# Performance work log

Hardware: AMD Instinct MI355X
Metric: run time of the kernel (lower is better)

The kernel has to match this reference:

```python
import jax, jax.numpy as jnp
import numpy as np

ALPHA = 0.1
BETA = 1.1
NUM_CLASSES = 16
EPS = 1e-8  # matches torch cosine_similarity eps
BATCH = 131072
DIM = 512


def setup_inputs() -> dict:
    key = jax.random.key(0)
    k1, k2 = jax.random.split(key)
    embeddings = jax.random.normal(k1, (BATCH, DIM), dtype=jnp.float32)
    labels = jax.random.randint(k2, (BATCH,), 0, NUM_CLASSES)
    return {"embeddings": embeddings, "labels": labels}


def _cos_dist(a, b):
    # a: [M, D], b: [N, D] -> 1 - cosine_similarity, shape [M, N]
    an = a / jnp.maximum(jnp.linalg.norm(a, axis=-1, keepdims=True), EPS)
    bn = b / jnp.maximum(jnp.linalg.norm(b, axis=-1, keepdims=True), EPS)
    return 1.0 - an @ bn.T


def reference(embeddings, labels):
    C = NUM_CLASSES
    N = embeddings.shape[0]
    dt = embeddings.dtype

    # class centroids (dummy anchors) via scatter-mean
    cnt = jax.ops.segment_sum(jnp.ones((N,), dt), labels, num_segments=C)  # [C]
    sums = jax.ops.segment_sum(embeddings, labels, num_segments=C)        # [C, D]
    centroids = sums / jnp.maximum(cnt, 1.0)[:, None]
    present = cnt > 0

    # close class pairs: i < j, both present, centroid distance <= beta
    pd = _cos_dist(centroids, centroids)                    # [C, C]
    upper = jnp.triu(jnp.ones((C, C), bool), k=1)
    pairmask = upper & (pd <= BETA) & present[:, None] & present[None, :]
    pm = pairmask.astype(dt)
    deg = pm.sum(1) + pm.sum(0)                             # pairs involving each class

    # distances from every centroid to every sample
    D = _cos_dist(centroids, embeddings)                    # [C, N]

    # intra: each sample of class c contributes relu(d(cent_c, x) - alpha),
    # once per close pair involving c
    d_own = D[labels, jnp.arange(N)]                        # [N]
    intra_sum = jnp.sum(deg[labels] * jax.nn.relu(d_own - ALPHA))

    # inter: S[c, c'] = sum over samples with label c' of relu(beta - d(cent_c, x))
    S = jax.ops.segment_sum(jax.nn.relu(BETA - D).T, labels, num_segments=C).T  # [C, C]
    inter_sum = jnp.sum(pm * (S + S.T))

    # number of terms in each loss list: sum over pairs of (cnt_i + cnt_j)
    count = jnp.sum(deg * cnt)
    denom = jnp.maximum(count, 1.0)
    num_pairs = pm.sum()

    loss = jnp.where(num_pairs > 0, intra_sum / denom + inter_sum / denom, 0.0)
    return loss
```

## Files before the change

kernel.cpp:

```cpp
#include <hip/hip_runtime.h>

constexpr float kAlpha = 0.1f;
constexpr float kBeta  = 1.1f;
constexpr int   kC     = 16;
constexpr int   kD     = 512;
constexpr float kEps   = 1e-8f;

constexpr int SUMS_OFF = 0;
constexpr int CNT_OFF  = 8192;
constexpr int TOT_OFF  = 8208;
constexpr int CN_OFF   = 8224;
constexpr int MSK_OFF  = 16416;
constexpr int SCL_OFF  = 16432;
constexpr int ZERO_FLOATS = 8209;

__global__ __launch_bounds__(512) void k1_sums(const float* __restrict__ emb,
                                               const int* __restrict__ labels,
                                               float* __restrict__ sums,
                                               float* __restrict__ cnt,
                                               int N, int rpb) {
    int tid = threadIdx.x;
    int myc = tid & 15;
    float acc[kC];
#pragma unroll
    for (int c = 0; c < kC; ++c) acc[c] = 0.f;
    float cacc = 0.f;

    int r0 = blockIdx.x * rpb;
    int r1 = min(r0 + rpb, N);
    int r = r0;
    for (; r + 8 <= r1; r += 8) {
        int4 la = *(const int4*)(labels + r);
        int4 lb = *(const int4*)(labels + r + 4);
        const float* e = emb + (size_t)r * kD + tid;
        float v0 = e[0 * kD];
        float v1 = e[1 * kD];
        float v2 = e[2 * kD];
        float v3 = e[3 * kD];
        float v4 = e[4 * kD];
        float v5 = e[5 * kD];
        float v6 = e[6 * kD];
        float v7 = e[7 * kD];
#pragma unroll
        for (int c = 0; c < kC; ++c) {
            float s = (la.x == c ? v0 : 0.f) + (la.y == c ? v1 : 0.f)
                    + (la.z == c ? v2 : 0.f) + (la.w == c ? v3 : 0.f)
                    + (lb.x == c ? v4 : 0.f) + (lb.y == c ? v5 : 0.f)
                    + (lb.z == c ? v6 : 0.f) + (lb.w == c ? v7 : 0.f);
            acc[c] += s;
        }
        cacc += (la.x == myc ? 1.f : 0.f) + (la.y == myc ? 1.f : 0.f)
              + (la.z == myc ? 1.f : 0.f) + (la.w == myc ? 1.f : 0.f)
              + (lb.x == myc ? 1.f : 0.f) + (lb.y == myc ? 1.f : 0.f)
              + (lb.z == myc ? 1.f : 0.f) + (lb.w == myc ? 1.f : 0.f);
    }
    for (; r < r1; ++r) {
        int l = labels[r];
        float v = emb[(size_t)r * kD + tid];
#pragma unroll
        for (int c = 0; c < kC; ++c) acc[c] += (l == c ? v : 0.f);
        cacc += (l == myc ? 1.f : 0.f);
    }

#pragma unroll
    for (int c = 0; c < kC; ++c) atomicAdd(&sums[c * kD + tid], acc[c]);
    if (tid < kC) atomicAdd(&cnt[tid], cacc);
}

__global__ __launch_bounds__(256) void k2_cent(const float* __restrict__ sums,
                                               const float* __restrict__ cnt_g,
                                               float* __restrict__ cn_g,
                                               unsigned* __restrict__ mask_g,
                                               float* __restrict__ scal) {
    __shared__ __align__(16) float lcn[kC * kD];
    __shared__ float lcnt[kC];
    __shared__ float red[256];
    __shared__ float norms[kC];
    __shared__ float pdm[kC * kC];
    int tid = threadIdx.x;
    if (tid < kC) lcnt[tid] = cnt_g[tid];
    __syncthreads();

    int c = tid >> 4, sub = tid & 15;
    float invc = 1.f / fmaxf(lcnt[c], 1.f);
    float sq = 0.f;
    for (int d = sub; d < kD; d += 16) {
        float v = sums[c * kD + d] * invc;
        lcn[c * kD + d] = v;
        sq += v * v;
    }
    red[tid] = sq;
    __syncthreads();
    if (tid < kC) {
        float t = 0.f;
        for (int k = 0; k < 16; ++k) t += red[tid * 16 + k];
        norms[tid] = fmaxf(sqrtf(t), kEps);
    }
    __syncthreads();
    for (int i = tid; i < kC * kD; i += 256) {
        float v = lcn[i] / norms[i / kD];
        lcn[i] = v;
        cn_g[i] = v;
    }
    __syncthreads();
    int pi = tid >> 4, pj = tid & 15;
    float dot = 0.f;
    for (int dd = 0; dd < kD; ++dd) {
        int d = (dd + tid) & (kD - 1);
        dot += lcn[pi * kD + d] * lcn[pj * kD + d];
    }
    pdm[tid] = 1.f - dot;
    __syncthreads();
    if (tid == 0) {
        unsigned m[kC];
        for (int a = 0; a < kC; ++a) m[a] = 0u;
        float npairs = 0.f;
        for (int a = 0; a < kC; ++a)
            for (int b = a + 1; b < kC; ++b) {
                bool close = (pdm[a * kC + b] <= kBeta) && (lcnt[a] > 0.f) && (lcnt[b] > 0.f);
                if (close) { m[a] |= 1u << b; m[b] |= 1u << a; npairs += 1.f; }
            }
        float count = 0.f;
        for (int a = 0; a < kC; ++a) {
            mask_g[a] = m[a];
            count += (float)__popc(m[a]) * lcnt[a];
        }
        scal[0] = fmaxf(count, 1.f);
        scal[1] = npairs;
    }
}

__global__ __launch_bounds__(256) void k3_main(const float* __restrict__ emb,
                                               const int* __restrict__ labels,
                                               const float* __restrict__ cn_g,
                                               const unsigned* __restrict__ mask_g,
                                               float* __restrict__ total,
                                               int N, int rpb) {
    __shared__ __align__(16) float lcn[kC * kD];
    __shared__ unsigned lmask[kC];
    __shared__ float wsum[4];
    int tid = threadIdx.x;
    for (int i = tid; i < kC * kD; i += 256) lcn[i] = cn_g[i];
    if (tid < kC) lmask[tid] = mask_g[tid];
    __syncthreads();

    const int j = tid & 15;
    const int grp = tid >> 4;
    const float4* w4 = (const float4*)lcn;

    float priv = 0.f;
    int r0 = blockIdx.x * rpb;
    int r1 = min(r0 + rpb, N);
    for (int rb = r0; rb < r1; rb += 16) {
        int r = rb + grp;
        bool valid = (r < r1);
        int rc = valid ? r : r0;
        int lab = labels[rc];
        const float4* x4 = (const float4*)(emb + (size_t)rc * kD);

        float dots[kC];
#pragma unroll
        for (int c = 0; c < kC; ++c) dots[c] = 0.f;
        float nrm = 0.f;

#pragma unroll
        for (int it = 0; it < kD / 64; ++it) {
            float4 x = x4[it * 16 + j];
            nrm += x.x * x.x + x.y * x.y + x.z * x.z + x.w * x.w;
#pragma unroll
            for (int c = 0; c < kC; ++c) {
                float4 w = w4[c * (kD / 4) + it * 16 + j];
                dots[c] += x.x * w.x + x.y * w.y + x.z * w.z + x.w * w.w;
            }
        }

#pragma unroll
        for (int m = 1; m < 16; m <<= 1) {
#pragma unroll
            for (int c = 0; c < kC; ++c) dots[c] += __shfl_xor(dots[c], m, 64);
            nrm += __shfl_xor(nrm, m, 64);
        }

        if (j == 0 && valid) {
            unsigned mm = lmask[lab];
            float inv = 1.f / fmaxf(sqrtf(nrm), kEps);
            float down = 0.f;
#pragma unroll
            for (int c = 0; c < kC; ++c) down = (c == lab) ? (1.f - dots[c] * inv) : down;
            float s = (float)__popc(mm) * fmaxf(down - kAlpha, 0.f);
#pragma unroll
            for (int c = 0; c < kC; ++c) {
                float dd = 1.f - dots[c] * inv;
                s += ((mm >> c) & 1u) ? fmaxf(kBeta - dd, 0.f) : 0.f;
            }
            priv += s;
        }
    }

#pragma unroll
    for (int off = 32; off > 0; off >>= 1) priv += __shfl_down(priv, off, 64);
    if ((tid & 63) == 0) wsum[tid >> 6] = priv;
    __syncthreads();
    if (tid == 0) atomicAdd(total, wsum[0] + wsum[1] + wsum[2] + wsum[3]);
}

__global__ void k4_final(const float* __restrict__ total,
                         const float* __restrict__ scal,
                         float* __restrict__ out) {
    out[0] = (scal[1] > 0.f) ? (total[0] / scal[0]) : 0.f;
}

extern "C" void kernel_launch(void* const* d_in, const int* in_sizes, int n_in,
                              void* d_out, int out_size, void* d_ws, size_t ws_size,
                              hipStream_t stream) {
    const float* emb = (const float*)d_in[0];
    const int* labels = (const int*)d_in[1];
    int N = in_sizes[0] / kD;

    float* ws = (float*)d_ws;
    float* sums = ws + SUMS_OFF;
    float* cnt = ws + CNT_OFF;
    float* total = ws + TOT_OFF;
    float* cn = ws + CN_OFF;
    unsigned* mask = (unsigned*)(ws + MSK_OFF);
    float* scal = ws + SCL_OFF;

    hipMemsetAsync(d_ws, 0, ZERO_FLOATS * sizeof(float), stream);

    int blocks1 = 512;
    int rpb1 = (N + blocks1 - 1) / blocks1;
    k1_sums<<<blocks1, 512, 0, stream>>>(emb, labels, sums, cnt, N, rpb1);

    k2_cent<<<1, 256, 0, stream>>>(sums, cnt, cn, mask, scal);

    int blocks3 = 512;
    int rpb3 = (N + blocks3 - 1) / blocks3;
    k3_main<<<blocks3, 256, 0, stream>>>(emb, labels, cn, mask, total, N, rpb3);

    k4_final<<<1, 1, 0, stream>>>(total, scal, (float*)d_out);
}
```

Baseline: 686.2 us.

## Keep centroids in registers and stage row tiles through LDS in distance kernel

New measurement: 557.2 us. 1.23x faster.

```diff
diff --git a/kernel.cpp b/kernel.cpp
--- a/kernel.cpp
+++ b/kernel.cpp
@@ -14,57 +14,66 @@
 constexpr int SCL_OFF  = 16432;
 constexpr int ZERO_FLOATS = 8209;
 
+__device__ __forceinline__ float dot4(float4 a, float4 b) {
+    return a.x * b.x + a.y * b.y + a.z * b.z + a.w * b.w;
+}
+
 __global__ __launch_bounds__(512) void k1_sums(const float* __restrict__ emb,
                                                const int* __restrict__ labels,
                                                float* __restrict__ sums,
                                                float* __restrict__ cnt,
                                                int N, int rpb) {
+    __shared__ float lacc[kC * kD];
+    __shared__ float lcnt[kC];
     int tid = threadIdx.x;
-    int myc = tid & 15;
-    float acc[kC];
-#pragma unroll
-    for (int c = 0; c < kC; ++c) acc[c] = 0.f;
+    int wave = tid >> 6, lane = tid & 63;
+    int half = wave & 1;
+
+    for (int i = tid; i < kC * kD; i += 512) lacc[i] = 0.f;
+    if (tid < kC) lcnt[tid] = 0.f;
+    __syncthreads();
+
+    float4 acc[kC];
+#pragma unroll
+    for (int c = 0; c < kC; ++c) acc[c] = make_float4(0.f, 0.f, 0.f, 0.f);
     float cacc = 0.f;
 
-    int r0 = blockIdx.x * rpb;
-    int r1 = min(r0 + rpb, N);
-    int r = r0;
-    for (; r + 8 <= r1; r += 8) {
-        int4 la = *(const int4*)(labels + r);
-        int4 lb = *(const int4*)(labels + r + 4);
-        const float* e = emb + (size_t)r * kD + tid;
-        float v0 = e[0 * kD];
-        float v1 = e[1 * kD];
-        float v2 = e[2 * kD];
-        float v3 = e[3 * kD];
-        float v4 = e[4 * kD];
-        float v5 = e[5 * kD];
-        float v6 = e[6 * kD];
-        float v7 = e[7 * kD];
+    const float4* e4 = (const float4*)emb;
+    long long h0 = 2LL * blockIdx.x * rpb;
+    long long hEnd = min(h0 + 2LL * rpb, 2LL * (long long)N);
+
+    for (long long h = h0 + wave; h < hEnd; h += 16) {
+        long long hb = h + 8;
+        bool vb = (hb < hEnd);
+        int rowA = (int)(h >> 1);
+        int rowB = vb ? (int)(hb >> 1) : rowA;
+        int lA = labels[rowA];
+        int lB = labels[rowB];
+        float4 vA = e4[(size_t)rowA * 128 + half * 64 + lane];
+        float4 vB = e4[(size_t)rowB * 128 + half * 64 + lane];
+        if (!vb) vB = make_float4(0.f, 0.f, 0.f, 0.f);
 #pragma unroll
         for (int c = 0; c < kC; ++c) {
-            float s = (la.x == c ? v0 : 0.f) + (la.y == c ? v1 : 0.f)
-                    + (la.z == c ? v2 : 0.f) + (la.w == c ? v3 : 0.f)
-                    + (lb.x == c ? v4 : 0.f) + (lb.y == c ? v5 : 0.f)
-                    + (lb.z == c ? v6 : 0.f) + (lb.w == c ? v7 : 0.f);
-            acc[c] += s;
-        }
-        cacc += (la.x == myc ? 1.f : 0.f) + (la.y == myc ? 1.f : 0.f)
-              + (la.z == myc ? 1.f : 0.f) + (la.w == myc ? 1.f : 0.f)
-              + (lb.x == myc ? 1.f : 0.f) + (lb.y == myc ? 1.f : 0.f)
-              + (lb.z == myc ? 1.f : 0.f) + (lb.w == myc ? 1.f : 0.f);
-    }
-    for (; r < r1; ++r) {
-        int l = labels[r];
-        float v = emb[(size_t)r * kD + tid];
-#pragma unroll
-        for (int c = 0; c < kC; ++c) acc[c] += (l == c ? v : 0.f);
-        cacc += (l == myc ? 1.f : 0.f);
-    }
-
-#pragma unroll
-    for (int c = 0; c < kC; ++c) atomicAdd(&sums[c * kD + tid], acc[c]);
-    if (tid < kC) atomicAdd(&cnt[tid], cacc);
+            if (lA == c) { acc[c].x += vA.x; acc[c].y += vA.y; acc[c].z += vA.z; acc[c].w += vA.w; }
+            if (lB == c) { acc[c].x += vB.x; acc[c].y += vB.y; acc[c].z += vB.z; acc[c].w += vB.w; }
+        }
+        if (half == 0 && lane < kC) {
+            cacc += (lA == lane ? 1.f : 0.f) + ((vb && lB == lane) ? 1.f : 0.f);
+        }
+    }
+
+#pragma unroll
+    for (int c = 0; c < kC; ++c) {
+        float* p = &lacc[c * kD + half * 256 + lane * 4];
+        atomicAdd(p + 0, acc[c].x);
+        atomicAdd(p + 1, acc[c].y);
+        atomicAdd(p + 2, acc[c].z);
+        atomicAdd(p + 3, acc[c].w);
+    }
+    if (half == 0 && lane < kC) atomicAdd(&lcnt[lane], cacc);
+    __syncthreads();
+    for (int i = tid; i < kC * kD; i += 512) atomicAdd(&sums[i], lacc[i]);
+    if (tid < kC) atomicAdd(&cnt[tid], lcnt[tid]);
 }
 
 __global__ __launch_bounds__(256) void k2_cent(const float* __restrict__ sums,
@@ -130,78 +139,116 @@
     }
 }
 
-__global__ __launch_bounds__(256) void k3_main(const float* __restrict__ emb,
-                                               const int* __restrict__ labels,
-                                               const float* __restrict__ cn_g,
-                                               const unsigned* __restrict__ mask_g,
-                                               float* __restrict__ total,
-                                               int N, int rpb) {
-    __shared__ __align__(16) float lcn[kC * kD];
+constexpr int TR = 32;
+__global__ __launch_bounds__(512, 2) void k3_main(const float* __restrict__ emb,
+                                                  const int* __restrict__ labels,
+                                                  const float* __restrict__ cn_g,
+                                                  const unsigned* __restrict__ mask_g,
+                                                  float* __restrict__ total,
+                                                  int N, int rpb) {
+    __shared__ __align__(16) float4 xbuf[TR * 128];
     __shared__ unsigned lmask[kC];
-    __shared__ float wsum[4];
+    __shared__ float wsum[8];
     int tid = threadIdx.x;
-    for (int i = tid; i < kC * kD; i += 256) lcn[i] = cn_g[i];
+    int wave = tid >> 6, lane = tid & 63;
+    int g = lane >> 4, j = lane & 15;
+
+    const float4* w4 = (const float4*)cn_g;
+    float4 wreg[4][8];
+#pragma unroll
+    for (int c = 0; c < 4; ++c)
+#pragma unroll
+        for (int i = 0; i < 8; ++i)
+            wreg[c][i] = w4[(4 * g + c) * 128 + i * 16 + j];
     if (tid < kC) lmask[tid] = mask_g[tid];
-    __syncthreads();
-
-    const int j = tid & 15;
-    const int grp = tid >> 4;
-    const float4* w4 = (const float4*)lcn;
-
-    float priv = 0.f;
+
     int r0 = blockIdx.x * rpb;
     int r1 = min(r0 + rpb, N);
-    for (int rb = r0; rb < r1; rb += 16) {
-        int r = rb + grp;
-        bool valid = (r < r1);
-        int rc = valid ? r : r0;
-        int lab = labels[rc];
-        const float4* x4 = (const float4*)(emb + (size_t)rc * kD);
-
-        float dots[kC];
-#pragma unroll
-        for (int c = 0; c < kC; ++c) dots[c] = 0.f;
-        float nrm = 0.f;
-
-#pragma unroll
-        for (int it = 0; it < kD / 64; ++it) {
-            float4 x = x4[it * 16 + j];
-            nrm += x.x * x.x + x.y * x.y + x.z * x.z + x.w * x.w;
-#pragma unroll
-            for (int c = 0; c < kC; ++c) {
-                float4 w = w4[c * (kD / 4) + it * 16 + j];
-                dots[c] += x.x * w.x + x.y * w.y + x.z * w.z + x.w * w.w;
-            }
-        }
-
-#pragma unroll
-        for (int m = 1; m < 16; m <<= 1) {
-#pragma unroll
-            for (int c = 0; c < kC; ++c) dots[c] += __shfl_xor(dots[c], m, 64);
-            nrm += __shfl_xor(nrm, m, 64);
-        }
-
-        if (j == 0 && valid) {
-            unsigned mm = lmask[lab];
-            float inv = 1.f / fmaxf(sqrtf(nrm), kEps);
-            float down = 0.f;
-#pragma unroll
-            for (int c = 0; c < kC; ++c) down = (c == lab) ? (1.f - dots[c] * inv) : down;
-            float s = (float)__popc(mm) * fmaxf(down - kAlpha, 0.f);
-#pragma unroll
-            for (int c = 0; c < kC; ++c) {
-                float dd = 1.f - dots[c] * inv;
-                s += ((mm >> c) & 1u) ? fmaxf(kBeta - dd, 0.f) : 0.f;
-            }
-            priv += s;
-        }
+    float priv = 0.f;
+
+    const float4* src = (const float4*)emb;
+    float4 st[8];
+
+    if (r0 < r1) {
+        int avail = (r1 - r0) * 128;
+#pragma unroll
+        for (int k = 0; k < 8; ++k) {
+            int idx = k * 512 + tid;
+            st[k] = (idx < avail) ? src[(size_t)r0 * 128 + idx] : make_float4(0.f, 0.f, 0.f, 0.f);
+        }
+#pragma unroll
+        for (int k = 0; k < 8; ++k) xbuf[k * 512 + tid] = st[k];
+    }
+    __syncthreads();
+
+    for (int rt = r0; rt < r1; rt += TR) {
+        int ntile = rt + TR;
+        bool more = (ntile < r1);
+        if (more) {
+            int avail = (r1 - ntile) * 128;
+#pragma unroll
+            for (int k = 0; k < 8; ++k) {
+                int idx = k * 512 + tid;
+                st[k] = (idx < avail) ? src[(size_t)ntile * 128 + idx] : make_float4(0.f, 0.f, 0.f, 0.f);
+            }
+        }
+
+        int rows = min(TR, r1 - rt);
+        for (int rr = wave; rr < rows; rr += 8) {
+            int row = rt + rr;
+            int lab = labels[row];
+            const float4* xr = &xbuf[rr * 128];
+            float d0 = 0.f, d1 = 0.f, d2 = 0.f, d3 = 0.f, nrm = 0.f;
+#pragma unroll
+            for (int i = 0; i < 8; ++i) {
+                float4 x = xr[i * 16 + j];
+                nrm += dot4(x, x);
+                d0 += dot4(x, wreg[0][i]);
+                d1 += dot4(x, wreg[1][i]);
+                d2 += dot4(x, wreg[2][i]);
+                d3 += dot4(x, wreg[3][i]);
+            }
+#pragma unroll
+            for (int m = 1; m < 16; m <<= 1) {
+                d0 += __shfl_xor(d0, m, 64);
+                d1 += __shfl_xor(d1, m, 64);
+                d2 += __shfl_xor(d2, m, 64);
+                d3 += __shfl_xor(d3, m, 64);
+                nrm += __shfl_xor(nrm, m, 64);
+            }
+            if (j == 0) {
+                unsigned mm = lmask[lab];
+                float inv = 1.f / fmaxf(sqrtf(nrm), kEps);
+                float s = 0.f;
+                float dv[4] = {d0, d1, d2, d3};
+#pragma unroll
+                for (int c = 0; c < 4; ++c) {
+                    int cg = 4 * g + c;
+                    float dd = 1.f - dv[c] * inv;
+                    if ((mm >> cg) & 1u) s += fmaxf(kBeta - dd, 0.f);
+                    if (cg == lab) s += (float)__popc(mm) * fmaxf(dd - kAlpha, 0.f);
+                }
+                priv += s;
+            }
+        }
+        __syncthreads();
+        if (more) {
+#pragma unroll
+            for (int k = 0; k < 8; ++k) xbuf[k * 512 + tid] = st[k];
+        }
+        __syncthreads();
     }
 
 #pragma unroll
     for (int off = 32; off > 0; off >>= 1) priv += __shfl_down(priv, off, 64);
-    if ((tid & 63) == 0) wsum[tid >> 6] = priv;
-    __syncthreads();
-    if (tid == 0) atomicAdd(total, wsum[0] + wsum[1] + wsum[2] + wsum[3]);
+    if (lane == 0) wsum[wave] = priv;
+    __syncthreads();
+    if (tid == 0) {
+        float t = 0.f;
+#pragma unroll
+        for (int w = 0; w < 8; ++w) t += wsum[w];
+        atomicAdd(total, t);
+    }
 }
 
 __global__ void k4_final(const float* __restrict__ total,
@@ -233,9 +280,9 @@
 
     k2_cent<<<1, 256, 0, stream>>>(sums, cnt, cn, mask, scal);
 
-    int blocks3 = 512;
+    int blocks3 = 256;
     int rpb3 = (N + blocks3 - 1) / blocks3;
-    k3_main<<<blocks3, 256, 0, stream>>>(emb, labels, cn, mask, total, N, rpb3);
+    k3_main<<<blocks3, 512, 0, stream>>>(emb, labels, cn, mask, total, N, rpb3);
 
     k4_final<<<1, 1, 0, stream>>>(total, scal, (float*)d_out);
 }
```
